# Kernel optimization log

Measured on AMD Instinct MI355X. Metric: run time of the kernel, lower is better.

The kernel has to match this reference:

```python
import jax, jax.numpy as jnp
import numpy as np

DT = 1.0 / 60.0  # physics timestep
NUM_BODY = 20

# ---- quaternion helpers (xyzw convention, matching the repo) ----

def quat_from_rotvec(rv):
    # rv: [..., 3] axis-angle -> quaternion [..., 4] (x,y,z,w)
    angle = jnp.linalg.norm(rv, axis=-1, keepdims=True)
    half = 0.5 * angle
    safe = jnp.where(angle < 1e-8, 1.0, angle)
    s = jnp.where(angle < 1e-8, 0.5 - angle * angle / 48.0, jnp.sin(half) / safe)
    return jnp.concatenate([rv * s, jnp.cos(half)], axis=-1)


def flip_quat_by_w(q):
    return jnp.where(q[..., 3:4] < 0, -q, q)


def quat_to_vec6d(q):
    # first two columns of the rotation matrix, row-major flattened -> [..., 6]
    x, y, z, w = q[..., 0], q[..., 1], q[..., 2], q[..., 3]
    r00 = 1 - 2 * (y * y + z * z)
    r10 = 2 * (x * y + z * w)
    r20 = 2 * (x * z - y * w)
    r01 = 2 * (x * y - z * w)
    r11 = 1 - 2 * (x * x + z * z)
    r21 = 2 * (y * z + x * w)
    return jnp.stack([r00, r01, r10, r11, r20, r21], axis=-1)


def quat_apply(q, v):
    # rotate v [..., 3] by quaternion q [..., 4]; broadcasts over leading dims
    xyz, w = q[..., :3], q[..., 3:4]
    t = 2.0 * jnp.cross(xyz, v)
    return v + w * t + jnp.cross(xyz, t)


def quat_multiply(p, q):
    pv, pw = p[..., :3], p[..., 3:4]
    qv, qw = q[..., :3], q[..., 3:4]
    v = pw * qv + qw * pv + jnp.cross(pv, qv)
    w = pw * qw - jnp.sum(pv * qv, axis=-1, keepdims=True)
    return jnp.concatenate([v, w], axis=-1)


def quat_integrate(q, omega, dt):
    # q_{t+1} = normalize(q + 0.5*dt * (omega_quat * q))
    omega_q = jnp.concatenate([omega, jnp.zeros_like(omega[..., :1])], axis=-1)
    dq = quat_multiply(omega_q, q)
    r = q + 0.5 * dt * dq
    return r / jnp.linalg.norm(r, axis=-1, keepdims=True)


def integrate_state(state, delta, dt):
    # state: [B, NB, 13] = pos(3) | rot quat(4) | vel(3) | avel(3)
    B, NB, _ = state.shape
    pos, rot = state[..., 0:3], state[..., 3:7]
    vel, avel = state[..., 7:10], state[..., 10:13]
    root_rot = state[:, 0:1, 3:7]                       # [B, 1, 4]
    d3 = delta.reshape(B, -1, 3)                        # [B, 2*NB, 3]
    true_d = quat_apply(root_rot, d3).reshape(B, NB, 6)
    lin, ang = true_d[..., :3], true_d[..., 3:]
    next_vel = vel + lin
    next_avel = avel + ang
    next_pos = pos + next_vel * dt
    next_rot = quat_integrate(rot, next_avel, dt)
    return jnp.concatenate([next_pos, next_rot, next_vel, next_avel], axis=-1)


def setup_inputs() -> dict:
    key = jax.random.key(0)
    ks = jax.random.split(key, 12)
    B = 32768
    inp = {
        "state": jax.random.normal(ks[0], (B, NUM_BODY, 13), jnp.float32),
        "action": jax.random.normal(ks[1], (B, 57), jnp.float32),
        "n_observation": jax.random.normal(ks[2], (B, 300), jnp.float32),
        "W1": jax.random.normal(ks[3], (414, 512), jnp.float32) * 0.05,
        "b1": jax.random.normal(ks[4], (512,), jnp.float32) * 0.05,
        "W2": jax.random.normal(ks[5], (512, 512), jnp.float32) * 0.05,
        "b2": jax.random.normal(ks[6], (512,), jnp.float32) * 0.05,
        "W3": jax.random.normal(ks[7], (512, 120), jnp.float32) * 0.05,
        "b3": jax.random.normal(ks[8], (120,), jnp.float32) * 0.05,
        "delta_mean": jax.random.normal(ks[9], (120,), jnp.float32) * 0.01,
        "delta_std": jax.random.uniform(ks[10], (120,), jnp.float32) + 0.5,
    }
    return inp


def reference(state, action, n_observation, W1, b1, W2, b2, W3, b3, delta_mean, delta_std):
    B = action.shape[0]
    # action rotvecs -> quats -> 6d representation
    aq = flip_quat_by_w(quat_from_rotvec(action.reshape(-1, 3)))
    a6 = quat_to_vec6d(aq).reshape(B, -1)               # [B, 114]
    x = jnp.concatenate([n_observation, a6], axis=-1)   # [B, 414]
    h = jax.nn.relu(x @ W1 + b1)
    h = jax.nn.relu(h @ W2 + b2)
    n_delta = h @ W3 + b3                                # [B, 120]
    delta = n_delta * delta_std + delta_mean             # unnormalize
    return integrate_state(state, delta, DT)
```

## Files before the change

kernel.cpp:

```cpp
#include <hip/hip_runtime.h>
#include <hip/hip_bf16.h>
#include <math.h>

#define DT (1.0f / 60.0f)

typedef __bf16 bf16x8 __attribute__((ext_vector_type(8)));
typedef float f32x4 __attribute__((ext_vector_type(4)));

#define XSTRIDE 848
#define HSTRIDE 1040

struct __attribute__((packed)) f4u {
    float x, y, z, w;
};

__global__ __launch_bounds__(256) void prep_weights(
    const float* __restrict__ W1, const float* __restrict__ W2,
    const float* __restrict__ W3, __hip_bfloat16* __restrict__ W1p,
    __hip_bfloat16* __restrict__ W2p, __hip_bfloat16* __restrict__ W3p) {
    int idx = blockIdx.x * 256 + threadIdx.x;
    if (idx < 212992) {
        int d = idx;
        int e = d & 7, l = (d >> 3) & 63, t = d >> 9;
        int nt = t & 31, ks = t >> 5;
        int n = nt * 16 + (l & 15);
        int k = ks * 32 + (l >> 4) * 8 + e;
        W1p[d] = __float2bfloat16(k < 414 ? W1[k * 512 + n] : 0.0f);
        return;
    }
    idx -= 212992;
    if (idx < 262144) {
        int d = idx;
        int e = d & 7, l = (d >> 3) & 63, t = d >> 9;
        int nt = t & 31, ks = t >> 5;
        int n = nt * 16 + (l & 15);
        int k = ks * 32 + (l >> 4) * 8 + e;
        W2p[d] = __float2bfloat16(W2[k * 512 + n]);
        return;
    }
    idx -= 262144;
    if (idx < 65536) {
        int d = idx;
        int e = d & 7, l = (d >> 3) & 63, t = d >> 9;
        int nt = t & 7, ks = t >> 3;
        int n = nt * 16 + (l & 15);
        int k = ks * 32 + (l >> 4) * 8 + e;
        W3p[d] = __float2bfloat16(n < 120 ? W3[k * 120 + n] : 0.0f);
    }
}

template <int KSTEPS, int NT, int ASTRIDE>
__device__ __forceinline__ void mlp_layer(const char* Abase, const char* Bbase,
                                          int laneOff, f32x4 (&acc)[4][8]) {
    bf16x8 w0[8], w1[8];
#pragma unroll
    for (int j = 0; j < 8; j++)
        w0[j] = *(const bf16x8*)(Bbase + (j << 10) + laneOff);
#pragma unroll 2
    for (int ks = 0; ks < KSTEPS; ks++) {
        if (ks + 1 < KSTEPS) {
            if ((ks & 1) == 0) {
#pragma unroll
                for (int j = 0; j < 8; j++)
                    w1[j] = *(const bf16x8*)(Bbase + (((ks + 1) * NT + j) << 10) + laneOff);
            } else {
#pragma unroll
                for (int j = 0; j < 8; j++)
                    w0[j] = *(const bf16x8*)(Bbase + (((ks + 1) * NT + j) << 10) + laneOff);
            }
        }
        bf16x8 ax[4];
#pragma unroll
        for (int i = 0; i < 4; i++)
            ax[i] = *(const bf16x8*)(Abase + ks * 64 + i * 16 * ASTRIDE);
#pragma unroll
        for (int i = 0; i < 4; i++)
#pragma unroll
            for (int j = 0; j < 8; j++)
                acc[i][j] = __builtin_amdgcn_mfma_f32_16x16x32_bf16(
                    (ks & 1) ? w1[j] : w0[j], ax[i], acc[i][j], 0, 0, 0);
    }
}

__device__ __forceinline__ void store_h_relu_t(const f32x4 (&acc)[4][8],
                                               char* smem, const float* bias,
                                               int wn, int lrow, int kgrp) {
#pragma unroll
    for (int j = 0; j < 8; j++) {
        int f = wn * 128 + j * 16 + kgrp * 4;
        float4 bb = *(const float4*)(bias + f);
#pragma unroll
        for (int i = 0; i < 4; i++) {
            float v0 = acc[i][j][0] + bb.x;
            float v1 = acc[i][j][1] + bb.y;
            float v2 = acc[i][j][2] + bb.z;
            float v3 = acc[i][j][3] + bb.w;
            v0 = v0 > 0.0f ? v0 : 0.0f;
            v1 = v1 > 0.0f ? v1 : 0.0f;
            v2 = v2 > 0.0f ? v2 : 0.0f;
            v3 = v3 > 0.0f ? v3 : 0.0f;
            union { __hip_bfloat162 h2[2]; uint2 u; } pk;
            pk.h2[0] = __float22bfloat162_rn(make_float2(v0, v1));
            pk.h2[1] = __float22bfloat162_rn(make_float2(v2, v3));
            *(uint2*)(smem + (i * 16 + lrow) * HSTRIDE + f * 2) = pk.u;
        }
    }
}

__device__ __forceinline__ void quat_apply3(float qx, float qy, float qz,
                                            float qw, float vx, float vy,
                                            float vz, float& ox, float& oy,
                                            float& oz) {
    float tx = 2.0f * (qy * vz - qz * vy);
    float ty = 2.0f * (qz * vx - qx * vz);
    float tz = 2.0f * (qx * vy - qy * vx);
    ox = vx + qw * tx + (qy * tz - qz * ty);
    oy = vy + qw * ty + (qz * tx - qx * tz);
    oz = vz + qw * tz + (qx * ty - qy * tx);
}

__global__ __launch_bounds__(256, 2) void fused_mlp(
    const float* __restrict__ obs, const float* __restrict__ action,
    const __hip_bfloat16* __restrict__ W1p, const float* __restrict__ b1,
    const __hip_bfloat16* __restrict__ W2p, const float* __restrict__ b2,
    const __hip_bfloat16* __restrict__ W3p, const float* __restrict__ b3,
    const float* __restrict__ dstd, const float* __restrict__ dmean,
    const float* __restrict__ state, float* __restrict__ out) {
    alignas(16) __shared__ char smem[64 * HSTRIDE];
    const int tid = threadIdx.x;
    const int blk = blockIdx.x;
    const int lane = tid & 63, wn = tid >> 6;
    const int lrow = lane & 15, kgrp = lane >> 4;
    const int laneOff = lane * 16;

    {
        const float4* og = (const float4*)obs + (size_t)blk * 64 * 75;
#pragma unroll
        for (int i = 0; i < 19; i++) {
            int f = tid + i * 256;
            if (f < 4800) {
                int row = f / 75;
                int c4 = f - row * 75;
                float4 v = og[f];
                union { __hip_bfloat162 h2[2]; uint2 u; } pk;
                pk.h2[0] = __float22bfloat162_rn(make_float2(v.x, v.y));
                pk.h2[1] = __float22bfloat162_rn(make_float2(v.z, v.w));
                *(uint2*)(smem + row * XSTRIDE + c4 * 8) = pk.u;
            }
        }
#pragma unroll
        for (int i = 0; i < 5; i++) {
            int q = tid + i * 256;
            if (q < 1216) {
                int row = q / 19;
                int j = q - row * 19;
                const float* a = action + ((size_t)(blk * 64 + row)) * 57 + j * 3;
                float rx = a[0], ry = a[1], rz = a[2];
                float ang = sqrtf(rx * rx + ry * ry + rz * rz);
                float half = 0.5f * ang;
                float s;
                if (ang < 1e-8f)
                    s = 0.5f - ang * ang * (1.0f / 48.0f);
                else
                    s = sinf(half) / ang;
                float qx = rx * s, qy = ry * s, qz = rz * s, qw = cosf(half);
                union { __hip_bfloat16 h[6]; uint u[3]; } pq;
                pq.h[0] = __float2bfloat16(1.0f - 2.0f * (qy * qy + qz * qz));
                pq.h[1] = __float2bfloat16(2.0f * (qx * qy - qz * qw));
                pq.h[2] = __float2bfloat16(2.0f * (qx * qy + qz * qw));
                pq.h[3] = __float2bfloat16(1.0f - 2.0f * (qx * qx + qz * qz));
                pq.h[4] = __float2bfloat16(2.0f * (qx * qz - qy * qw));
                pq.h[5] = __float2bfloat16(2.0f * (qy * qz + qx * qw));
                char* p = smem + row * XSTRIDE + 600 + j * 12;
                *(uint*)p = pq.u[0];
                *(uint*)(p + 4) = pq.u[1];
                *(uint*)(p + 8) = pq.u[2];
            }
        }
#pragma unroll
        for (int i = 0; i < 2; i++) {
            int id = tid + i * 256;
            if (id < 320) {
                int row = id / 5;
                int p = id - row * 5;
                *(uint*)(smem + row * XSTRIDE + 828 + p * 4) = 0u;
            }
        }
    }
    __syncthreads();

    f32x4 acc[4][8];
    f32x4 zero4 = {0.0f, 0.0f, 0.0f, 0.0f};
#pragma unroll
    for (int i = 0; i < 4; i++)
#pragma unroll
        for (int j = 0; j < 8; j++) acc[i][j] = zero4;

    mlp_layer<13, 32, XSTRIDE>(smem + lrow * XSTRIDE + kgrp * 16,
                               (const char*)W1p + (wn << 13), laneOff, acc);
    __syncthreads();
    store_h_relu_t(acc, smem, b1, wn, lrow, kgrp);
    __syncthreads();

#pragma unroll
    for (int i = 0; i < 4; i++)
#pragma unroll
        for (int j = 0; j < 8; j++) acc[i][j] = zero4;
    mlp_layer<16, 32, HSTRIDE>(smem + lrow * HSTRIDE + kgrp * 16,
                               (const char*)W2p + (wn << 13), laneOff, acc);
    __syncthreads();
    store_h_relu_t(acc, smem, b2, wn, lrow, kgrp);
    __syncthreads();

    f4u ps0[5], ps1[5], ps2[5], prq[5];
    float ps12[5];
#pragma unroll
    for (int it = 0; it < 5; it++) {
        int idx = tid + it * 256;
        int lr = idx / 20;
        int body = idx - lr * 20;
        const float* sb = state + ((size_t)(blk * 64 + lr)) * 260 + body * 13;
        const float* rq = state + ((size_t)(blk * 64 + lr)) * 260 + 3;
        ps0[it] = *(const f4u*)sb;
        ps1[it] = *(const f4u*)(sb + 4);
        ps2[it] = *(const f4u*)(sb + 8);
        ps12[it] = sb[12];
        prq[it] = *(const f4u*)rq;
    }

    f32x4 a3[4][2];
#pragma unroll
    for (int i = 0; i < 4; i++)
#pragma unroll
        for (int j = 0; j < 2; j++) a3[i][j] = zero4;
    {
        const char* Ab = smem + lrow * HSTRIDE + kgrp * 16;
        const char* Bb = (const char*)W3p;
        bf16x8 c0[2], c1[2];
#pragma unroll
        for (int j = 0; j < 2; j++)
            c0[j] = *(const bf16x8*)(Bb + ((wn * 2 + j) << 10) + laneOff);
#pragma unroll 2
        for (int ks = 0; ks < 16; ks++) {
            if (ks + 1 < 16) {
                if ((ks & 1) == 0) {
#pragma unroll
                    for (int j = 0; j < 2; j++)
                        c1[j] = *(const bf16x8*)(Bb + (((ks + 1) * 8 + wn * 2 + j) << 10) + laneOff);
                } else {
#pragma unroll
                    for (int j = 0; j < 2; j++)
                        c0[j] = *(const bf16x8*)(Bb + (((ks + 1) * 8 + wn * 2 + j) << 10) + laneOff);
                }
            }
            bf16x8 ax[4];
#pragma unroll
            for (int i = 0; i < 4; i++)
                ax[i] = *(const bf16x8*)(Ab + ks * 64 + i * 16 * HSTRIDE);
#pragma unroll
            for (int i = 0; i < 4; i++)
#pragma unroll
                for (int j = 0; j < 2; j++)
                    a3[i][j] = __builtin_amdgcn_mfma_f32_16x16x32_bf16(
                        (ks & 1) ? c1[j] : c0[j], ax[i], a3[i][j], 0, 0, 0);
        }
    }
    __syncthreads();

    float* dl = (float*)smem;
#pragma unroll
    for (int j = 0; j < 2; j++) {
        int f = wn * 32 + j * 16 + kgrp * 4;
        if (f < 120) {
            float4 bb = *(const float4*)(b3 + f);
            float4 sc = *(const float4*)(dstd + f);
            float4 mn = *(const float4*)(dmean + f);
#pragma unroll
            for (int i = 0; i < 4; i++) {
                int row = i * 16 + lrow;
                float4 dv;
                dv.x = (a3[i][j][0] + bb.x) * sc.x + mn.x;
                dv.y = (a3[i][j][1] + bb.y) * sc.y + mn.y;
                dv.z = (a3[i][j][2] + bb.z) * sc.z + mn.z;
                dv.w = (a3[i][j][3] + bb.w) * sc.w + mn.w;
                *(float4*)(dl + row * 120 + f) = dv;
            }
        }
    }
    __syncthreads();

#pragma unroll
    for (int it = 0; it < 5; it++) {
        int idx = tid + it * 256;
        int lr = idx / 20;
        int body = idx - lr * 20;
        int rowg = blk * 64 + lr;
        float qx = prq[it].x, qy = prq[it].y, qz = prq[it].z, qw = prq[it].w;
        const float* d = dl + lr * 120 + body * 6;

        float lx, ly, lz, ax, ay, az;
        quat_apply3(qx, qy, qz, qw, d[0], d[1], d[2], lx, ly, lz);
        quat_apply3(qx, qy, qz, qw, d[3], d[4], d[5], ax, ay, az);

        float vx = ps1[it].w + lx, vy = ps2[it].x + ly, vz = ps2[it].y + lz;
        float wx = ps2[it].z + ax, wy = ps2[it].w + ay, wz = ps12[it] + az;
        float px = ps0[it].x + vx * DT, py = ps0[it].y + vy * DT,
              pz = ps0[it].z + vz * DT;

        float rx = ps0[it].w, ry = ps1[it].x, rz = ps1[it].y, rw = ps1[it].z;
        float dqx = rw * wx + (wy * rz - wz * ry);
        float dqy = rw * wy + (wz * rx - wx * rz);
        float dqz = rw * wz + (wx * ry - wy * rx);
        float dqw = -(wx * rx + wy * ry + wz * rz);
        float h = 0.5f * DT;
        float nx = rx + h * dqx, ny = ry + h * dqy, nz = rz + h * dqz,
              nw = rw + h * dqw;
        float inv = 1.0f / sqrtf(nx * nx + ny * ny + nz * nz + nw * nw);

        float* o = out + (size_t)rowg * 260 + body * 13;
        o[0] = px;
        o[1] = py;
        o[2] = pz;
        o[3] = nx * inv;
        o[4] = ny * inv;
        o[5] = nz * inv;
        o[6] = nw * inv;
        o[7] = vx;
        o[8] = vy;
        o[9] = vz;
        o[10] = wx;
        o[11] = wy;
        o[12] = wz;
    }
}

extern "C" void kernel_launch(void* const* d_in, const int* in_sizes, int n_in,
                              void* d_out, int out_size, void* d_ws,
                              size_t ws_size, hipStream_t stream) {
    const float* state = (const float*)d_in[0];
    const float* action = (const float*)d_in[1];
    const float* obs = (const float*)d_in[2];
    const float* W1 = (const float*)d_in[3];
    const float* b1 = (const float*)d_in[4];
    const float* W2 = (const float*)d_in[5];
    const float* b2 = (const float*)d_in[6];
    const float* W3 = (const float*)d_in[7];
    const float* b3 = (const float*)d_in[8];
    const float* dmean = (const float*)d_in[9];
    const float* dstd = (const float*)d_in[10];
    float* out = (float*)d_out;
    char* ws = (char*)d_ws;

    const int B = in_sizes[1] / 57;

    __hip_bfloat16* W1p = (__hip_bfloat16*)(ws);
    __hip_bfloat16* W2p = (__hip_bfloat16*)(ws + 425984);
    __hip_bfloat16* W3p = (__hip_bfloat16*)(ws + 950272);

    prep_weights<<<2112, 256, 0, stream>>>(W1, W2, W3, W1p, W2p, W3p);
    fused_mlp<<<B / 64, 256, 0, stream>>>(obs, action, W1p, b1, W2p, b2, W3p,
                                          b3, dstd, dmean, state, out);
}
```

Baseline: 165.3 us.

## Split MLP across 8 waves per block with smaller per-wave N tiles

Doubles the block from 4 to 8 waves so each wave computes 64 output columns instead of 128 (and one 16-column tile of layer 3 instead of two). This halves accumulator registers per wave, which should allow more resident waves. It also removes the register double-buffered weight prefetch, and the state loads are no longer issued early before layer 3 but read directly in the epilogue. The trade-off is that the activation tile in shared memory is read twice as many times overall, and weight-load latency is now exposed instead of hidden by the prefetch.

```diff
diff --git a/kernel.cpp b/kernel.cpp
--- a/kernel.cpp
+++ b/kernel.cpp
@@ -9,10 +9,6 @@
 
 #define XSTRIDE 848
 #define HSTRIDE 1040
-
-struct __attribute__((packed)) f4u {
-    float x, y, z, w;
-};
 
 __global__ __launch_bounds__(256) void prep_weights(
     const float* __restrict__ W1, const float* __restrict__ W2,
@@ -51,24 +47,12 @@
 
 template <int KSTEPS, int NT, int ASTRIDE>
 __device__ __forceinline__ void mlp_layer(const char* Abase, const char* Bbase,
-                                          int laneOff, f32x4 (&acc)[4][8]) {
-    bf16x8 w0[8], w1[8];
-#pragma unroll
-    for (int j = 0; j < 8; j++)
-        w0[j] = *(const bf16x8*)(Bbase + (j << 10) + laneOff);
-#pragma unroll 2
+                                          f32x4 (&acc)[4][4]) {
     for (int ks = 0; ks < KSTEPS; ks++) {
-        if (ks + 1 < KSTEPS) {
-            if ((ks & 1) == 0) {
-#pragma unroll
-                for (int j = 0; j < 8; j++)
-                    w1[j] = *(const bf16x8*)(Bbase + (((ks + 1) * NT + j) << 10) + laneOff);
-            } else {
-#pragma unroll
-                for (int j = 0; j < 8; j++)
-                    w0[j] = *(const bf16x8*)(Bbase + (((ks + 1) * NT + j) << 10) + laneOff);
-            }
-        }
+        bf16x8 w[4];
+#pragma unroll
+        for (int j = 0; j < 4; j++)
+            w[j] = *(const bf16x8*)(Bbase + ((ks * NT + j) << 10));
         bf16x8 ax[4];
 #pragma unroll
         for (int i = 0; i < 4; i++)
@@ -76,18 +60,18 @@
 #pragma unroll
         for (int i = 0; i < 4; i++)
 #pragma unroll
-            for (int j = 0; j < 8; j++)
+            for (int j = 0; j < 4; j++)
                 acc[i][j] = __builtin_amdgcn_mfma_f32_16x16x32_bf16(
-                    (ks & 1) ? w1[j] : w0[j], ax[i], acc[i][j], 0, 0, 0);
-    }
-}
-
-__device__ __forceinline__ void store_h_relu_t(const f32x4 (&acc)[4][8],
+                    w[j], ax[i], acc[i][j], 0, 0, 0);
+    }
+}
+
+__device__ __forceinline__ void store_h_relu_t(const f32x4 (&acc)[4][4],
                                                char* smem, const float* bias,
                                                int wn, int lrow, int kgrp) {
 #pragma unroll
-    for (int j = 0; j < 8; j++) {
-        int f = wn * 128 + j * 16 + kgrp * 4;
+    for (int j = 0; j < 4; j++) {
+        int f = wn * 64 + j * 16 + kgrp * 4;
         float4 bb = *(const float4*)(bias + f);
 #pragma unroll
         for (int i = 0; i < 4; i++) {
@@ -119,7 +103,7 @@
     oz = vz + qw * tz + (qx * ty - qy * tx);
 }
 
-__global__ __launch_bounds__(256, 2) void fused_mlp(
+__global__ __launch_bounds__(512, 2) void fused_mlp(
     const float* __restrict__ obs, const float* __restrict__ action,
     const __hip_bfloat16* __restrict__ W1p, const float* __restrict__ b1,
     const __hip_bfloat16* __restrict__ W2p, const float* __restrict__ b2,
@@ -136,8 +120,8 @@
     {
         const float4* og = (const float4*)obs + (size_t)blk * 64 * 75;
 #pragma unroll
-        for (int i = 0; i < 19; i++) {
-            int f = tid + i * 256;
+        for (int i = 0; i < 10; i++) {
+            int f = tid + i * 512;
             if (f < 4800) {
                 int row = f / 75;
                 int c4 = f - row * 75;
@@ -149,8 +133,8 @@
             }
         }
 #pragma unroll
-        for (int i = 0; i < 5; i++) {
-            int q = tid + i * 256;
+        for (int i = 0; i < 3; i++) {
+            int q = tid + i * 512;
             if (q < 1216) {
                 int row = q / 19;
                 int j = q - row * 19;
@@ -177,27 +161,23 @@
                 *(uint*)(p + 8) = pq.u[2];
             }
         }
-#pragma unroll
-        for (int i = 0; i < 2; i++) {
-            int id = tid + i * 256;
-            if (id < 320) {
-                int row = id / 5;
-                int p = id - row * 5;
-                *(uint*)(smem + row * XSTRIDE + 828 + p * 4) = 0u;
-            }
-        }
-    }
-    __syncthreads();
-
-    f32x4 acc[4][8];
+        if (tid < 320) {
+            int row = tid / 5;
+            int p = tid - row * 5;
+            *(uint*)(smem + row * XSTRIDE + 828 + p * 4) = 0u;
+        }
+    }
+    __syncthreads();
+
+    f32x4 acc[4][4];
     f32x4 zero4 = {0.0f, 0.0f, 0.0f, 0.0f};
 #pragma unroll
     for (int i = 0; i < 4; i++)
 #pragma unroll
-        for (int j = 0; j < 8; j++) acc[i][j] = zero4;
+        for (int j = 0; j < 4; j++) acc[i][j] = zero4;
 
     mlp_layer<13, 32, XSTRIDE>(smem + lrow * XSTRIDE + kgrp * 16,
-                               (const char*)W1p + (wn << 13), laneOff, acc);
+                               (const char*)W1p + (wn << 12) + laneOff, acc);
     __syncthreads();
     store_h_relu_t(acc, smem, b1, wn, lrow, kgrp);
     __syncthreads();
@@ -205,72 +185,36 @@
 #pragma unroll
     for (int i = 0; i < 4; i++)
 #pragma unroll
-        for (int j = 0; j < 8; j++) acc[i][j] = zero4;
+        for (int j = 0; j < 4; j++) acc[i][j] = zero4;
     mlp_layer<16, 32, HSTRIDE>(smem + lrow * HSTRIDE + kgrp * 16,
-                               (const char*)W2p + (wn << 13), laneOff, acc);
+                               (const char*)W2p + (wn << 12) + laneOff, acc);
     __syncthreads();
     store_h_relu_t(acc, smem, b2, wn, lrow, kgrp);
     __syncthreads();
 
-    f4u ps0[5], ps1[5], ps2[5], prq[5];
-    float ps12[5];
-#pragma unroll
-    for (int it = 0; it < 5; it++) {
-        int idx = tid + it * 256;
-        int lr = idx / 20;
-        int body = idx - lr * 20;
-        const float* sb = state + ((size_t)(blk * 64 + lr)) * 260 + body * 13;
-        const float* rq = state + ((size_t)(blk * 64 + lr)) * 260 + 3;
-        ps0[it] = *(const f4u*)sb;
-        ps1[it] = *(const f4u*)(sb + 4);
-        ps2[it] = *(const f4u*)(sb + 8);
-        ps12[it] = sb[12];
-        prq[it] = *(const f4u*)rq;
-    }
-
-    f32x4 a3[4][2];
-#pragma unroll
-    for (int i = 0; i < 4; i++)
-#pragma unroll
-        for (int j = 0; j < 2; j++) a3[i][j] = zero4;
+    f32x4 a3[4];
+#pragma unroll
+    for (int i = 0; i < 4; i++) a3[i] = zero4;
     {
         const char* Ab = smem + lrow * HSTRIDE + kgrp * 16;
-        const char* Bb = (const char*)W3p;
-        bf16x8 c0[2], c1[2];
-#pragma unroll
-        for (int j = 0; j < 2; j++)
-            c0[j] = *(const bf16x8*)(Bb + ((wn * 2 + j) << 10) + laneOff);
-#pragma unroll 2
+        const char* Bb = (const char*)W3p + (wn << 10) + laneOff;
         for (int ks = 0; ks < 16; ks++) {
-            if (ks + 1 < 16) {
-                if ((ks & 1) == 0) {
-#pragma unroll
-                    for (int j = 0; j < 2; j++)
-                        c1[j] = *(const bf16x8*)(Bb + (((ks + 1) * 8 + wn * 2 + j) << 10) + laneOff);
-                } else {
-#pragma unroll
-                    for (int j = 0; j < 2; j++)
-                        c0[j] = *(const bf16x8*)(Bb + (((ks + 1) * 8 + wn * 2 + j) << 10) + laneOff);
-                }
-            }
+            bf16x8 c = *(const bf16x8*)(Bb + (ks << 13));
             bf16x8 ax[4];
 #pragma unroll
             for (int i = 0; i < 4; i++)
                 ax[i] = *(const bf16x8*)(Ab + ks * 64 + i * 16 * HSTRIDE);
 #pragma unroll
             for (int i = 0; i < 4; i++)
-#pragma unroll
-                for (int j = 0; j < 2; j++)
-                    a3[i][j] = __builtin_amdgcn_mfma_f32_16x16x32_bf16(
-                        (ks & 1) ? c1[j] : c0[j], ax[i], a3[i][j], 0, 0, 0);
+                a3[i] = __builtin_amdgcn_mfma_f32_16x16x32_bf16(c, ax[i],
+                                                                a3[i], 0, 0, 0);
         }
     }
     __syncthreads();
 
     float* dl = (float*)smem;
-#pragma unroll
-    for (int j = 0; j < 2; j++) {
-        int f = wn * 32 + j * 16 + kgrp * 4;
+    {
+        int f = wn * 16 + kgrp * 4;
         if (f < 120) {
             float4 bb = *(const float4*)(b3 + f);
             float4 sc = *(const float4*)(dstd + f);
@@ -279,10 +223,10 @@
             for (int i = 0; i < 4; i++) {
                 int row = i * 16 + lrow;
                 float4 dv;
-                dv.x = (a3[i][j][0] + bb.x) * sc.x + mn.x;
-                dv.y = (a3[i][j][1] + bb.y) * sc.y + mn.y;
-                dv.z = (a3[i][j][2] + bb.z) * sc.z + mn.z;
-                dv.w = (a3[i][j][3] + bb.w) * sc.w + mn.w;
+                dv.x = (a3[i][0] + bb.x) * sc.x + mn.x;
+                dv.y = (a3[i][1] + bb.y) * sc.y + mn.y;
+                dv.z = (a3[i][2] + bb.z) * sc.z + mn.z;
+                dv.w = (a3[i][3] + bb.w) * sc.w + mn.w;
                 *(float4*)(dl + row * 120 + f) = dv;
             }
         }
@@ -290,47 +234,51 @@
     __syncthreads();
 
 #pragma unroll
-    for (int it = 0; it < 5; it++) {
-        int idx = tid + it * 256;
-        int lr = idx / 20;
-        int body = idx - lr * 20;
-        int rowg = blk * 64 + lr;
-        float qx = prq[it].x, qy = prq[it].y, qz = prq[it].z, qw = prq[it].w;
-        const float* d = dl + lr * 120 + body * 6;
-
-        float lx, ly, lz, ax, ay, az;
-        quat_apply3(qx, qy, qz, qw, d[0], d[1], d[2], lx, ly, lz);
-        quat_apply3(qx, qy, qz, qw, d[3], d[4], d[5], ax, ay, az);
-
-        float vx = ps1[it].w + lx, vy = ps2[it].x + ly, vz = ps2[it].y + lz;
-        float wx = ps2[it].z + ax, wy = ps2[it].w + ay, wz = ps12[it] + az;
-        float px = ps0[it].x + vx * DT, py = ps0[it].y + vy * DT,
-              pz = ps0[it].z + vz * DT;
-
-        float rx = ps0[it].w, ry = ps1[it].x, rz = ps1[it].y, rw = ps1[it].z;
-        float dqx = rw * wx + (wy * rz - wz * ry);
-        float dqy = rw * wy + (wz * rx - wx * rz);
-        float dqz = rw * wz + (wx * ry - wy * rx);
-        float dqw = -(wx * rx + wy * ry + wz * rz);
-        float h = 0.5f * DT;
-        float nx = rx + h * dqx, ny = ry + h * dqy, nz = rz + h * dqz,
-              nw = rw + h * dqw;
-        float inv = 1.0f / sqrtf(nx * nx + ny * ny + nz * nz + nw * nw);
-
-        float* o = out + (size_t)rowg * 260 + body * 13;
-        o[0] = px;
-        o[1] = py;
-        o[2] = pz;
-        o[3] = nx * inv;
-        o[4] = ny * inv;
-        o[5] = nz * inv;
-        o[6] = nw * inv;
-        o[7] = vx;
-        o[8] = vy;
-        o[9] = vz;
-        o[10] = wx;
-        o[11] = wy;
-        o[12] = wz;
+    for (int it = 0; it < 3; it++) {
+        int idx = tid + it * 512;
+        if (idx < 1280) {
+            int lr = idx / 20;
+            int body = idx - lr * 20;
+            int rowg = blk * 64 + lr;
+            const float* sb = state + (size_t)rowg * 260 + body * 13;
+            const float* rq = state + (size_t)rowg * 260 + 3;
+            float qx = rq[0], qy = rq[1], qz = rq[2], qw = rq[3];
+            const float* d = dl + lr * 120 + body * 6;
+
+            float lx, ly, lz, ax, ay, az;
+            quat_apply3(qx, qy, qz, qw, d[0], d[1], d[2], lx, ly, lz);
+            quat_apply3(qx, qy, qz, qw, d[3], d[4], d[5], ax, ay, az);
+
+            float vx = sb[7] + lx, vy = sb[8] + ly, vz = sb[9] + lz;
+            float wx = sb[10] + ax, wy = sb[11] + ay, wz = sb[12] + az;
+            float px = sb[0] + vx * DT, py = sb[1] + vy * DT,
+                  pz = sb[2] + vz * DT;
+
+            float rx = sb[3], ry = sb[4], rz = sb[5], rw = sb[6];
+            float dqx = rw * wx + (wy * rz - wz * ry);
+            float dqy = rw * wy + (wz * rx - wx * rz);
+            float dqz = rw * wz + (wx * ry - wy * rx);
+            float dqw = -(wx * rx + wy * ry + wz * rz);
+            float h = 0.5f * DT;
+            float nx = rx + h * dqx, ny = ry + h * dqy, nz = rz + h * dqz,
+                  nw = rw + h * dqw;
+            float inv = 1.0f / sqrtf(nx * nx + ny * ny + nz * nz + nw * nw);
+
+            float* o = out + (size_t)rowg * 260 + body * 13;
+            o[0] = px;
+            o[1] = py;
+            o[2] = pz;
+            o[3] = nx * inv;
+            o[4] = ny * inv;
+            o[5] = nz * inv;
+            o[6] = nw * inv;
+            o[7] = vx;
+            o[8] = vy;
+            o[9] = vz;
+            o[10] = wx;
+            o[11] = wy;
+            o[12] = wz;
+        }
     }
 }
 
@@ -358,6 +306,6 @@
     __hip_bfloat16* W3p = (__hip_bfloat16*)(ws + 950272);
 
     prep_weights<<<2112, 256, 0, stream>>>(W1, W2, W3, W1p, W2p, W3p);
-    fused_mlp<<<B / 64, 256, 0, stream>>>(obs, action, W1p, b1, W2p, b2, W3p,
+    fused_mlp<<<B / 64, 512, 0, stream>>>(obs, action, W1p, b1, W2p, b2, W3p,
                                           b3, dstd, dmean, state, out);
 }
```

Result: slower. 180.5 us (+9.2%).
